# Optimization experiments

Measured on AMD Instinct MI355X. Metric: run time of the kernel, lower is better.

## Reference

```python
import jax, jax.numpy as jnp
import numpy as np
from numpy.lib.stride_tricks import sliding_window_view

# Static configuration matching init_kwargs
F_, H_, W_ = 2, 32, 32          # video_shape
K = 5                            # kernel_size (odd)
HEADS, DIM_HEAD = 8, 64
N = F_ * H_ * W_                 # number of video tokens (2048)
PAD = K // 2
INNER = HEADS * DIM_HEAD         # 512


def _neighbors():
    # Flattened token index at each (f,h,w); pad with sentinel N (out of bounds -> zeros / masked)
    idx = np.arange(N, dtype=np.int32).reshape(F_, H_, W_)
    padded = np.full((F_ + 2 * PAD, H_ + 2 * PAD, W_ + 2 * PAD), N, dtype=np.int32)
    padded[PAD:PAD + F_, PAD:PAD + H_, PAD:PAD + W_] = idx
    # sliding_window_view matches unfoldNd's kernel-offset ordering (kf, kh, kw row-major)
    return sliding_window_view(padded, (K, K, K)).reshape(N, K ** 3)


NBR = jnp.asarray(_neighbors())                                   # [N, K^3]
# causal: query i attends only to neighbors with index <= i; prepend BOS column (never masked)
CAUSAL = jnp.pad(jnp.arange(N)[:, None] < NBR, ((0, 0), (1, 0)))  # [N, K^3 + 1]


def setup_inputs() -> dict:
    key = jax.random.key(0)
    k1, k2, k3 = jax.random.split(key, 3)
    return {
        "x": jax.random.normal(k1, (1, N, INNER), jnp.float32),
        "w_qkv": jax.random.normal(k2, (INNER, 3 * INNER), jnp.float32) * 0.02,
        "w_out": jax.random.normal(k3, (INNER, INNER), jnp.float32) * 0.02,
        "b_out": jnp.zeros((INNER,), jnp.float32),
    }


def reference(x, w_qkv, w_out, b_out):
    b, n, dim = x.shape            # n == N
    bh = b * HEADS
    scale = DIM_HEAD ** -0.5

    xp = jnp.pad(x, ((0, 0), (0, 1), (0, 0)))        # pad one zero token at the end: [b, n+1, dim]
    qkv = xp @ w_qkv                                  # [b, n+1, 3*inner]
    q, kk, vv = jnp.split(qkv, 3, axis=-1)

    def split_heads(t):  # 'b n (h d) -> (b h) n d'
        return t.reshape(b, n + 1, HEADS, DIM_HEAD).transpose(0, 2, 1, 3).reshape(bh, n + 1, DIM_HEAD)

    q, kk, vv = map(split_heads, (q, kk, vv))
    q = q[:, 1:] * scale                              # drop BOS query: [bh, n, d]
    k_bos, kk = kk[:, :1], kk[:, 1:]                  # BOS kv + n spatial tokens
    v_bos, vv = vv[:, :1], vv[:, 1:]

    # Append a zero row so the sentinel index N gathers zeros (== unfold's zero padding)
    zero = jnp.zeros((bh, 1, DIM_HEAD), kk.dtype)
    kw = jnp.concatenate([kk, zero], axis=1)[:, NBR]  # [bh, n, K^3, d]
    vw = jnp.concatenate([vv, zero], axis=1)[:, NBR]

    bos_k = jnp.broadcast_to(k_bos[:, None], (bh, n, 1, DIM_HEAD))
    bos_v = jnp.broadcast_to(v_bos[:, None], (bh, n, 1, DIM_HEAD))
    kw = jnp.concatenate([bos_k, kw], axis=2)         # [bh, n, K^3+1, d]
    vw = jnp.concatenate([bos_v, vw], axis=2)

    sim = jnp.einsum('bid,bijd->bij', q, kw)          # [bh, n, K^3+1]
    sim = jnp.where(CAUSAL[:n], -jnp.finfo(sim.dtype).max, sim)
    attn = jax.nn.softmax(sim, axis=-1)
    out = jnp.einsum('bij,bijd->bid', attn, vw)       # [bh, n, d]

    out = jnp.concatenate([v_bos, out], axis=1)       # BOS output = its value: [bh, n+1, d]
    out = out.reshape(b, HEADS, n + 1, DIM_HEAD).transpose(0, 2, 1, 3).reshape(b, n + 1, INNER)
    return (out @ w_out + b_out)[:, :n]
```

## Files before the change

### kernel.cpp

```cpp
#include <hip/hip_runtime.h>
#include <hip/hip_bf16.h>

#define NTOK  2048
#define INNER 512
#define KDIM  512
#define QKVP  1536

typedef __attribute__((ext_vector_type(8))) short bf16x8;
typedef __attribute__((ext_vector_type(4))) float f32x4;

__device__ __forceinline__ unsigned short f2b(float f) {
  unsigned int u = __float_as_uint(f);
  return (unsigned short)((u + 0x7FFFu + ((u >> 16) & 1u)) >> 16);
}

__global__ __launch_bounds__(256) void prep_w(const float* __restrict__ w_qkv,
                                              const float* __restrict__ w_out,
                                              unsigned short* __restrict__ wqkvT,
                                              unsigned short* __restrict__ woutT) {
  __shared__ float tile[32][33];
  int b = blockIdx.x;
  const float* in; unsigned short* out; int K, N, bx, by;
  if (b < 768) { in = w_qkv; out = wqkvT; K = 512; N = 1536; bx = b % 48; by = b / 48; }
  else { b -= 768; in = w_out; out = woutT; K = 512; N = 512; bx = b & 15; by = b >> 4; }
  const int k0 = by * 32, n0 = bx * 32;
  const int r = threadIdx.x >> 3, c4 = (threadIdx.x & 7) * 4;
  float4 v = *(const float4*)(in + (size_t)(k0 + r) * N + n0 + c4);
  tile[r][c4 + 0] = v.x; tile[r][c4 + 1] = v.y;
  tile[r][c4 + 2] = v.z; tile[r][c4 + 3] = v.w;
  __syncthreads();
  ushort4 o;
  o.x = f2b(tile[c4 + 0][r]);
  o.y = f2b(tile[c4 + 1][r]);
  o.z = f2b(tile[c4 + 2][r]);
  o.w = f2b(tile[c4 + 3][r]);
  *(ushort4*)(out + (size_t)(n0 + r) * K + k0 + c4) = o;
}

__global__ __launch_bounds__(256, 2) void gemm_qkv(const float* __restrict__ x,
                                                   const unsigned short* __restrict__ Bt,
                                                   unsigned short* __restrict__ C) {
  constexpr int BM = 64, BN = 128, BK = 32, N = 1536, K = 512;
  __shared__ __align__(16) unsigned short As[BM * BK];
  __shared__ __align__(16) unsigned short Bs[BN * BK];
  const int tid = threadIdx.x, lane = tid & 63, wave = tid >> 6;
  const int m0 = blockIdx.y * BM, n0 = blockIdx.x * BN;
  const int wm = (wave >> 1) * 32, wn = (wave & 1) * 64;
  const int ar = tid >> 2, ac = (tid & 3) * 8;
  const int li0 = tid * 8, li1 = (256 + tid) * 8;
  const int br0 = li0 >> 5, bc0 = li0 & 31;
  const int br1 = li1 >> 5, bc1 = li1 & 31;
  const int fr = lane & 15, fk = (lane >> 4) * 8;

  f32x4 acc[2][4] = {};

  for (int k0 = 0; k0 < K; k0 += BK) {
    float4 a0 = *(const float4*)(x + (size_t)(m0 + ar) * K + k0 + ac);
    float4 a1 = *(const float4*)(x + (size_t)(m0 + ar) * K + k0 + ac + 4);
    bf16x8 av;
    av[0] = (short)f2b(a0.x); av[1] = (short)f2b(a0.y);
    av[2] = (short)f2b(a0.z); av[3] = (short)f2b(a0.w);
    av[4] = (short)f2b(a1.x); av[5] = (short)f2b(a1.y);
    av[6] = (short)f2b(a1.z); av[7] = (short)f2b(a1.w);
    *(bf16x8*)&As[ar * BK + ac] = av;
    *(bf16x8*)&Bs[li0] = *(const bf16x8*)(Bt + (size_t)(n0 + br0) * K + k0 + bc0);
    *(bf16x8*)&Bs[li1] = *(const bf16x8*)(Bt + (size_t)(n0 + br1) * K + k0 + bc1);
    __syncthreads();

    bf16x8 af[2], bfr[4];
#pragma unroll
    for (int i = 0; i < 2; ++i) af[i] = *(const bf16x8*)&As[(wm + i * 16 + fr) * BK + fk];
#pragma unroll
    for (int j = 0; j < 4; ++j) bfr[j] = *(const bf16x8*)&Bs[(wn + j * 16 + fr) * BK + fk];
#pragma unroll
    for (int i = 0; i < 2; ++i)
#pragma unroll
      for (int j = 0; j < 4; ++j)
        acc[i][j] = __builtin_amdgcn_mfma_f32_16x16x32_bf16(af[i], bfr[j], acc[i][j], 0, 0, 0);
    __syncthreads();
  }

  const int er = (lane >> 4) * 4, ec = lane & 15;
#pragma unroll
  for (int i = 0; i < 2; ++i)
#pragma unroll
    for (int j = 0; j < 4; ++j) {
      const int col = n0 + wn + j * 16 + ec;
#pragma unroll
      for (int r = 0; r < 4; ++r) {
        const int row = m0 + wm + i * 16 + er + r;
        C[(size_t)row * N + col] = f2b(acc[i][j][r]);
      }
    }
}

__global__ __launch_bounds__(256, 2) void gemm_out(const unsigned short* __restrict__ A,
                                                   const unsigned short* __restrict__ Bt,
                                                   const float* __restrict__ bias,
                                                   float* __restrict__ C) {
  constexpr int BM = 64, BN = 64, BK = 32, N = 512, K = 512;
  __shared__ __align__(16) unsigned short As[BM * BK];
  __shared__ __align__(16) unsigned short Bs[BN * BK];
  const int tid = threadIdx.x, lane = tid & 63, wave = tid >> 6;
  const int m0 = blockIdx.y * BM, n0 = blockIdx.x * BN;
  const int wm = (wave >> 1) * 32, wn = (wave & 1) * 32;
  const int r = tid >> 2, c = (tid & 3) * 8, li = tid * 8;
  const int fr = lane & 15, fk = (lane >> 4) * 8;

  f32x4 acc[2][2] = {};

  for (int k0 = 0; k0 < K; k0 += BK) {
    *(bf16x8*)&As[li] = *(const bf16x8*)(A + (size_t)(m0 + r) * K + k0 + c);
    *(bf16x8*)&Bs[li] = *(const bf16x8*)(Bt + (size_t)(n0 + r) * K + k0 + c);
    __syncthreads();
    bf16x8 af[2], bfr[2];
#pragma unroll
    for (int i = 0; i < 2; ++i) af[i] = *(const bf16x8*)&As[(wm + i * 16 + fr) * BK + fk];
#pragma unroll
    for (int j = 0; j < 2; ++j) bfr[j] = *(const bf16x8*)&Bs[(wn + j * 16 + fr) * BK + fk];
#pragma unroll
    for (int i = 0; i < 2; ++i)
#pragma unroll
      for (int j = 0; j < 2; ++j)
        acc[i][j] = __builtin_amdgcn_mfma_f32_16x16x32_bf16(af[i], bfr[j], acc[i][j], 0, 0, 0);
    __syncthreads();
  }

  const int er = (lane >> 4) * 4, ec = lane & 15;
#pragma unroll
  for (int i = 0; i < 2; ++i)
#pragma unroll
    for (int j = 0; j < 2; ++j) {
      const int col = n0 + wn + j * 16 + ec;
      const float b = bias[col];
#pragma unroll
      for (int rr = 0; rr < 4; ++rr) {
        const int row = m0 + wm + i * 16 + er + rr;
        C[(size_t)row * N + col] = acc[i][j][rr] + b;
      }
    }
}

__global__ __launch_bounds__(512) void attn_mfma(const unsigned short* __restrict__ qkv,
                                                 unsigned short* __restrict__ O) {
  __shared__ __align__(16) int list[192];
  __shared__ int cntS;
  __shared__ __align__(16) float mOd[4][16][72];
  __shared__ float mM[4][16], mL[4][16];

  const int tid = threadIdx.x;
  const int hg = blockIdx.y;

  if (blockIdx.x == 128) {
    if (tid < 256) O[hg * 256 + tid] = qkv[1024 + hg * 256 + tid];
    return;
  }
  const int pt = blockIdx.x;
  const int f  = pt >> 6;
  const int hh = (pt >> 1) & 31;
  const int w0 = (pt & 1) << 4;
  const int base_i = (f << 10) | (hh << 5) | w0;

  if (tid < 192) list[tid] = 0x7FFFFFFF;
  if (tid == 0) { list[0] = 0; cntS = 1; }
  __syncthreads();
  if (tid >= 1 && tid <= 160) {
    int cc = tid - 1;
    int p = cc / 20, wo = cc - p * 20;
    int ff = (p < 5) ? 0 : 1;
    int h2 = hh - 2 + ((p < 5) ? p : (p - 5));
    bool ok = (p < 5) ? ((f == 1) ? (h2 >= 0 && h2 <= 31) : (p <= 2 && h2 >= 0))
                      : (f == 1 && h2 >= 0);
    if (ok) {
      bool diag = (ff == f) && (h2 == hh);
      int wlo = max(0, w0 - 2);
      int whi = min(31, diag ? (w0 + 15) : (w0 + 17));
      int w2 = wlo + wo;
      if (w2 <= whi) {
        int pos = atomicAdd(&cntS, 1);
        list[pos] = ((ff << 10) | (h2 << 5) | w2) + 1;
      }
    }
  }
  __syncthreads();
  const int cnt  = cntS;
  const int nsub = (cnt + 15) >> 4;

  const int lane = tid & 63;
  const int wave = tid >> 6;
  const int hw   = wave >> 1;
  const int half = wave & 1;
  const int head = hg * 4 + hw;
  const int quad = lane >> 4;
  const int ec   = lane & 15;

  const int i_q = base_i + ec;
  const int tq  = min(i_q + 1, 2047);
  const unsigned short* qrow = qkv + (size_t)tq * QKVP + head * 64 + quad * 8;
  const bf16x8 qb0 = *(const bf16x8*)(qrow);
  const bf16x8 qb1 = *(const bf16x8*)(qrow + 32);

  f32x4 Od[4] = {{0,0,0,0},{0,0,0,0},{0,0,0,0},{0,0,0,0}};
  float m = -1e30f, l = 0.0f;

  for (int sub = half; sub < nsub; sub += 2) {
    const int base = sub * 16;
    const int tok_e = list[base + ec];
    const int4 tokv = *(const int4*)&list[base + quad * 4];
    const int tk[4] = {tokv.x, tokv.y, tokv.z, tokv.w};

    f32x4 S = {0, 0, 0, 0};
    {
      const int t0 = (tok_e > 2047) ? 0 : tok_e;
      const unsigned short* kr = qkv + (size_t)t0 * QKVP + 512 + head * 64 + quad * 8;
      const bf16x8 kf0 = *(const bf16x8*)(kr);
      const bf16x8 kf1 = *(const bf16x8*)(kr + 32);
      S = __builtin_amdgcn_mfma_f32_16x16x32_bf16(kf0, qb0, S, 0, 0, 0);
      S = __builtin_amdgcn_mfma_f32_16x16x32_bf16(kf1, qb1, S, 0, 0, 0);
    }

    float Sm[4];
#pragma unroll
    for (int r = 0; r < 4; ++r) {
      const int tok = tk[r];
      const int idx = tok - 1;
      const bool v = (tok == 0) ||
                     ((idx <= i_q) && ((unsigned)((idx & 31) - (w0 + ec) + 2) <= 4u));
      Sm[r] = v ? S[r] * 0.125f : -1e30f;
    }
    float mx = fmaxf(fmaxf(Sm[0], Sm[1]), fmaxf(Sm[2], Sm[3]));
    mx = fmaxf(mx, __shfl_xor(mx, 16, 64));
    mx = fmaxf(mx, __shfl_xor(mx, 32, 64));
    const float mn = fmaxf(m, mx);
    const float corr = __expf(m - mn);
    m = mn;
    const float p0 = __expf(Sm[0] - mn);
    const float p1 = __expf(Sm[1] - mn);
    const float p2 = __expf(Sm[2] - mn);
    const float p3 = __expf(Sm[3] - mn);
    float rs = (p0 + p1) + (p2 + p3);
    rs += __shfl_xor(rs, 16, 64);
    rs += __shfl_xor(rs, 32, 64);
    l = l * corr + rs;

    bf16x8 pf;
    pf[0] = (short)f2b(p0); pf[1] = (short)f2b(p1);
    pf[2] = (short)f2b(p2); pf[3] = (short)f2b(p3);
    pf[4] = 0; pf[5] = 0; pf[6] = 0; pf[7] = 0;

    const unsigned short* vp[4];
#pragma unroll
    for (int j = 0; j < 4; ++j) {
      const int tv = (tk[j] > 2047) ? 0 : tk[j];
      vp[j] = qkv + (size_t)tv * QKVP + 1024 + head * 64 + ec;
    }
#pragma unroll
    for (int dt = 0; dt < 4; ++dt) {
      bf16x8 vf;
#pragma unroll
      for (int j = 0; j < 4; ++j) vf[j] = (short)vp[j][dt * 16];
      vf[4] = 0; vf[5] = 0; vf[6] = 0; vf[7] = 0;
#pragma unroll
      for (int r = 0; r < 4; ++r) Od[dt][r] *= corr;
      Od[dt] = __builtin_amdgcn_mfma_f32_16x16x32_bf16(vf, pf, Od[dt], 0, 0, 0);
    }
  }

  if (half == 1) {
#pragma unroll
    for (int dt = 0; dt < 4; ++dt)
      *(f32x4*)&mOd[hw][ec][dt * 16 + quad * 4] = Od[dt];
    if (quad == 0) { mM[hw][ec] = m; mL[hw][ec] = l; }
  }
  __syncthreads();
  if (half == 0 && i_q <= 2046) {
    const float m1 = mM[hw][ec], l1 = mL[hw][ec];
    const float mm = fmaxf(m, m1);
    const float c0 = __expf(m - mm), c1 = __expf(m1 - mm);
    const float rl = 1.0f / (l * c0 + l1 * c1);
    unsigned short* ob = O + (size_t)(i_q + 1) * 512 + head * 64 + quad * 4;
#pragma unroll
    for (int dt = 0; dt < 4; ++dt) {
      const f32x4 o1 = *(const f32x4*)&mOd[hw][ec][dt * 16 + quad * 4];
      ushort4 u;
      u.x = f2b((Od[dt][0] * c0 + o1[0] * c1) * rl);
      u.y = f2b((Od[dt][1] * c0 + o1[1] * c1) * rl);
      u.z = f2b((Od[dt][2] * c0 + o1[2] * c1) * rl);
      u.w = f2b((Od[dt][3] * c0 + o1[3] * c1) * rl);
      *(ushort4*)(ob + dt * 16) = u;
    }
  }
}


extern "C" void kernel_launch(void* const* d_in, const int* in_sizes, int n_in,
                              void* d_out, int out_size, void* d_ws, size_t ws_size,
                              hipStream_t stream) {
  const float* x     = (const float*)d_in[0];
  const float* w_qkv = (const float*)d_in[1];
  const float* w_out = (const float*)d_in[2];
  const float* b_out = (const float*)d_in[3];
  float* out = (float*)d_out;

  char* ws = (char*)d_ws;
  unsigned short* qkvb  = (unsigned short*)(ws);
  unsigned short* wqkvT = (unsigned short*)(ws + 6291456);
  unsigned short* woutT = (unsigned short*)(ws + 7864320);
  unsigned short* Ob    = (unsigned short*)(ws + 8388608);

  hipLaunchKernelGGL(prep_w, dim3(1024), dim3(256), 0, stream, w_qkv, w_out, wqkvT, woutT);

  hipLaunchKernelGGL(gemm_qkv, dim3(12, 32), dim3(256), 0, stream, x, wqkvT, qkvb);

  hipLaunchKernelGGL(attn_mfma, dim3(129, 2), dim3(512), 0, stream, qkvb, Ob);

  hipLaunchKernelGGL(gemm_out, dim3(8, 32), dim3(256), 0, stream, Ob, woutT, b_out, out);
}
```

Measured before the change: 98.38 us.

## Precompute neighbor lists in prep, async LDS loads in GEMMs, smaller attention blocks

Moves the per-tile neighbor-list construction out of the attention kernel into the weight-prep kernel, which writes the lists and counts to workspace for the attention kernel to load. Both GEMMs now fill B tiles (and A tiles for the output GEMM) with global_load_lds direct-to-LDS copies. The attention grid changes from 129x2 blocks of 512 threads to 129x4 blocks of 256 threads, handling two heads per block instead of four. Together these aim to shorten the attention kernel's serial prologue, raise block count for occupancy, and cut register staging in the GEMMs. The costs are an extra global round trip for the lists and reliance on the async copy finishing before the barrier.

```diff
diff --git a/kernel.cpp b/kernel.cpp
--- a/kernel.cpp
+++ b/kernel.cpp
@@ -14,152 +14,46 @@
   return (unsigned short)((u + 0x7FFFu + ((u >> 16) & 1u)) >> 16);
 }
 
-__global__ __launch_bounds__(256) void prep_w(const float* __restrict__ w_qkv,
-                                              const float* __restrict__ w_out,
-                                              unsigned short* __restrict__ wqkvT,
-                                              unsigned short* __restrict__ woutT) {
+__device__ __forceinline__ void async_copy16(const unsigned short* g, unsigned short* l) {
+  __builtin_amdgcn_global_load_lds((const __attribute__((address_space(1))) void*)g,
+                                   (__attribute__((address_space(3))) void*)l, 16, 0, 0);
+}
+
+__global__ __launch_bounds__(256) void prep(const float* __restrict__ w_qkv,
+                                            const float* __restrict__ w_out,
+                                            unsigned short* __restrict__ wqkvT,
+                                            unsigned short* __restrict__ woutT,
+                                            int* __restrict__ glist,
+                                            int* __restrict__ gcnt) {
   __shared__ float tile[32][33];
+  __shared__ int list[192];
+  __shared__ int cntS;
+  const int tid = threadIdx.x;
   int b = blockIdx.x;
-  const float* in; unsigned short* out; int K, N, bx, by;
-  if (b < 768) { in = w_qkv; out = wqkvT; K = 512; N = 1536; bx = b % 48; by = b / 48; }
-  else { b -= 768; in = w_out; out = woutT; K = 512; N = 512; bx = b & 15; by = b >> 4; }
-  const int k0 = by * 32, n0 = bx * 32;
-  const int r = threadIdx.x >> 3, c4 = (threadIdx.x & 7) * 4;
-  float4 v = *(const float4*)(in + (size_t)(k0 + r) * N + n0 + c4);
-  tile[r][c4 + 0] = v.x; tile[r][c4 + 1] = v.y;
-  tile[r][c4 + 2] = v.z; tile[r][c4 + 3] = v.w;
-  __syncthreads();
-  ushort4 o;
-  o.x = f2b(tile[c4 + 0][r]);
-  o.y = f2b(tile[c4 + 1][r]);
-  o.z = f2b(tile[c4 + 2][r]);
-  o.w = f2b(tile[c4 + 3][r]);
-  *(ushort4*)(out + (size_t)(n0 + r) * K + k0 + c4) = o;
-}
-
-__global__ __launch_bounds__(256, 2) void gemm_qkv(const float* __restrict__ x,
-                                                   const unsigned short* __restrict__ Bt,
-                                                   unsigned short* __restrict__ C) {
-  constexpr int BM = 64, BN = 128, BK = 32, N = 1536, K = 512;
-  __shared__ __align__(16) unsigned short As[BM * BK];
-  __shared__ __align__(16) unsigned short Bs[BN * BK];
-  const int tid = threadIdx.x, lane = tid & 63, wave = tid >> 6;
-  const int m0 = blockIdx.y * BM, n0 = blockIdx.x * BN;
-  const int wm = (wave >> 1) * 32, wn = (wave & 1) * 64;
-  const int ar = tid >> 2, ac = (tid & 3) * 8;
-  const int li0 = tid * 8, li1 = (256 + tid) * 8;
-  const int br0 = li0 >> 5, bc0 = li0 & 31;
-  const int br1 = li1 >> 5, bc1 = li1 & 31;
-  const int fr = lane & 15, fk = (lane >> 4) * 8;
-
-  f32x4 acc[2][4] = {};
-
-  for (int k0 = 0; k0 < K; k0 += BK) {
-    float4 a0 = *(const float4*)(x + (size_t)(m0 + ar) * K + k0 + ac);
-    float4 a1 = *(const float4*)(x + (size_t)(m0 + ar) * K + k0 + ac + 4);
-    bf16x8 av;
-    av[0] = (short)f2b(a0.x); av[1] = (short)f2b(a0.y);
-    av[2] = (short)f2b(a0.z); av[3] = (short)f2b(a0.w);
-    av[4] = (short)f2b(a1.x); av[5] = (short)f2b(a1.y);
-    av[6] = (short)f2b(a1.z); av[7] = (short)f2b(a1.w);
-    *(bf16x8*)&As[ar * BK + ac] = av;
-    *(bf16x8*)&Bs[li0] = *(const bf16x8*)(Bt + (size_t)(n0 + br0) * K + k0 + bc0);
-    *(bf16x8*)&Bs[li1] = *(const bf16x8*)(Bt + (size_t)(n0 + br1) * K + k0 + bc1);
-    __syncthreads();
-
-    bf16x8 af[2], bfr[4];
-#pragma unroll
-    for (int i = 0; i < 2; ++i) af[i] = *(const bf16x8*)&As[(wm + i * 16 + fr) * BK + fk];
-#pragma unroll
-    for (int j = 0; j < 4; ++j) bfr[j] = *(const bf16x8*)&Bs[(wn + j * 16 + fr) * BK + fk];
-#pragma unroll
-    for (int i = 0; i < 2; ++i)
-#pragma unroll
-      for (int j = 0; j < 4; ++j)
-        acc[i][j] = __builtin_amdgcn_mfma_f32_16x16x32_bf16(af[i], bfr[j], acc[i][j], 0, 0, 0);
-    __syncthreads();
-  }
-
-  const int er = (lane >> 4) * 4, ec = lane & 15;
-#pragma unroll
-  for (int i = 0; i < 2; ++i)
-#pragma unroll
-    for (int j = 0; j < 4; ++j) {
-      const int col = n0 + wn + j * 16 + ec;
-#pragma unroll
-      for (int r = 0; r < 4; ++r) {
-        const int row = m0 + wm + i * 16 + er + r;
-        C[(size_t)row * N + col] = f2b(acc[i][j][r]);
-      }
-    }
-}
-
-__global__ __launch_bounds__(256, 2) void gemm_out(const unsigned short* __restrict__ A,
-                                                   const unsigned short* __restrict__ Bt,
-                                                   const float* __restrict__ bias,
-                                                   float* __restrict__ C) {
-  constexpr int BM = 64, BN = 64, BK = 32, N = 512, K = 512;
-  __shared__ __align__(16) unsigned short As[BM * BK];
-  __shared__ __align__(16) unsigned short Bs[BN * BK];
-  const int tid = threadIdx.x, lane = tid & 63, wave = tid >> 6;
-  const int m0 = blockIdx.y * BM, n0 = blockIdx.x * BN;
-  const int wm = (wave >> 1) * 32, wn = (wave & 1) * 32;
-  const int r = tid >> 2, c = (tid & 3) * 8, li = tid * 8;
-  const int fr = lane & 15, fk = (lane >> 4) * 8;
-
-  f32x4 acc[2][2] = {};
-
-  for (int k0 = 0; k0 < K; k0 += BK) {
-    *(bf16x8*)&As[li] = *(const bf16x8*)(A + (size_t)(m0 + r) * K + k0 + c);
-    *(bf16x8*)&Bs[li] = *(const bf16x8*)(Bt + (size_t)(n0 + r) * K + k0 + c);
-    __syncthreads();
-    bf16x8 af[2], bfr[2];
-#pragma unroll
-    for (int i = 0; i < 2; ++i) af[i] = *(const bf16x8*)&As[(wm + i * 16 + fr) * BK + fk];
-#pragma unroll
-    for (int j = 0; j < 2; ++j) bfr[j] = *(const bf16x8*)&Bs[(wn + j * 16 + fr) * BK + fk];
-#pragma unroll
-    for (int i = 0; i < 2; ++i)
-#pragma unroll
-      for (int j = 0; j < 2; ++j)
-        acc[i][j] = __builtin_amdgcn_mfma_f32_16x16x32_bf16(af[i], bfr[j], acc[i][j], 0, 0, 0);
-    __syncthreads();
-  }
-
-  const int er = (lane >> 4) * 4, ec = lane & 15;
-#pragma unroll
-  for (int i = 0; i < 2; ++i)
-#pragma unroll
-    for (int j = 0; j < 2; ++j) {
-      const int col = n0 + wn + j * 16 + ec;
-      const float b = bias[col];
-#pragma unroll
-      for (int rr = 0; rr < 4; ++rr) {
-        const int row = m0 + wm + i * 16 + er + rr;
-        C[(size_t)row * N + col] = acc[i][j][rr] + b;
-      }
-    }
-}
-
-__global__ __launch_bounds__(512) void attn_mfma(const unsigned short* __restrict__ qkv,
-                                                 unsigned short* __restrict__ O) {
-  __shared__ __align__(16) int list[192];
-  __shared__ int cntS;
-  __shared__ __align__(16) float mOd[4][16][72];
-  __shared__ float mM[4][16], mL[4][16];
-
-  const int tid = threadIdx.x;
-  const int hg = blockIdx.y;
-
-  if (blockIdx.x == 128) {
-    if (tid < 256) O[hg * 256 + tid] = qkv[1024 + hg * 256 + tid];
+
+  if (b < 1024) {
+    const float* in; unsigned short* out; int K, N, bx, by;
+    if (b < 768) { in = w_qkv; out = wqkvT; K = 512; N = 1536; bx = b % 48; by = b / 48; }
+    else { int bb = b - 768; in = w_out; out = woutT; K = 512; N = 512; bx = bb & 15; by = bb >> 4; }
+    const int k0 = by * 32, n0 = bx * 32;
+    const int r = tid >> 3, c4 = (tid & 7) * 4;
+    float4 v = *(const float4*)(in + (size_t)(k0 + r) * N + n0 + c4);
+    tile[r][c4 + 0] = v.x; tile[r][c4 + 1] = v.y;
+    tile[r][c4 + 2] = v.z; tile[r][c4 + 3] = v.w;
+    __syncthreads();
+    ushort4 o;
+    o.x = f2b(tile[c4 + 0][r]);
+    o.y = f2b(tile[c4 + 1][r]);
+    o.z = f2b(tile[c4 + 2][r]);
+    o.w = f2b(tile[c4 + 3][r]);
+    *(ushort4*)(out + (size_t)(n0 + r) * K + k0 + c4) = o;
     return;
   }
-  const int pt = blockIdx.x;
+
+  const int pt = b - 1024;
   const int f  = pt >> 6;
   const int hh = (pt >> 1) & 31;
   const int w0 = (pt & 1) << 4;
-  const int base_i = (f << 10) | (hh << 5) | w0;
 
   if (tid < 192) list[tid] = 0x7FFFFFFF;
   if (tid == 0) { list[0] = 0; cntS = 1; }
@@ -183,6 +77,141 @@
     }
   }
   __syncthreads();
+  if (tid < 192) glist[pt * 192 + tid] = list[tid];
+  if (tid == 0) gcnt[pt] = cntS;
+}
+
+__global__ __launch_bounds__(256, 2) void gemm_qkv(const float* __restrict__ x,
+                                                   const unsigned short* __restrict__ Bt,
+                                                   unsigned short* __restrict__ C) {
+  constexpr int BK = 32, N = 1536, K = 512;
+  __shared__ __align__(16) unsigned short As[64 * BK];
+  __shared__ __align__(16) unsigned short Bs[128 * BK];
+  const int tid = threadIdx.x, lane = tid & 63, wave = tid >> 6;
+  const int m0 = blockIdx.y * 64, n0 = blockIdx.x * 128;
+  const int wm = (wave >> 1) * 32, wn = (wave & 1) * 64;
+  const int ar = tid >> 2, ac = (tid & 3) * 8;
+  const int bl0 = ((wave * 2 + 0) * 64 + lane) * 8;
+  const int bl1 = ((wave * 2 + 1) * 64 + lane) * 8;
+  const int bn0 = bl0 >> 5, bk0 = bl0 & 31;
+  const int bn1 = bl1 >> 5, bk1 = bl1 & 31;
+  const int fr = lane & 15, fk = (lane >> 4) * 8;
+
+  f32x4 acc[2][4] = {};
+
+  for (int k0 = 0; k0 < K; k0 += BK) {
+    async_copy16(Bt + (size_t)(n0 + bn0) * K + k0 + bk0, &Bs[bl0]);
+    async_copy16(Bt + (size_t)(n0 + bn1) * K + k0 + bk1, &Bs[bl1]);
+    const float* ap = x + (size_t)(m0 + ar) * K + k0 + ac;
+    float4 a0 = *(const float4*)(ap);
+    float4 a1 = *(const float4*)(ap + 4);
+    bf16x8 av;
+    av[0] = (short)f2b(a0.x); av[1] = (short)f2b(a0.y);
+    av[2] = (short)f2b(a0.z); av[3] = (short)f2b(a0.w);
+    av[4] = (short)f2b(a1.x); av[5] = (short)f2b(a1.y);
+    av[6] = (short)f2b(a1.z); av[7] = (short)f2b(a1.w);
+    *(bf16x8*)&As[ar * BK + ac] = av;
+    __syncthreads();
+
+    bf16x8 af[2], bfr[4];
+#pragma unroll
+    for (int i = 0; i < 2; ++i) af[i] = *(const bf16x8*)&As[(wm + i * 16 + fr) * BK + fk];
+#pragma unroll
+    for (int j = 0; j < 4; ++j) bfr[j] = *(const bf16x8*)&Bs[(wn + j * 16 + fr) * BK + fk];
+#pragma unroll
+    for (int i = 0; i < 2; ++i)
+#pragma unroll
+      for (int j = 0; j < 4; ++j)
+        acc[i][j] = __builtin_amdgcn_mfma_f32_16x16x32_bf16(af[i], bfr[j], acc[i][j], 0, 0, 0);
+    __syncthreads();
+  }
+
+  const int er = (lane >> 4) * 4, ec = lane & 15;
+#pragma unroll
+  for (int i = 0; i < 2; ++i)
+#pragma unroll
+    for (int j = 0; j < 4; ++j) {
+      const int col = n0 + wn + j * 16 + ec;
+#pragma unroll
+      for (int r = 0; r < 4; ++r) {
+        const int row = m0 + wm + i * 16 + er + r;
+        C[(size_t)row * N + col] = f2b(acc[i][j][r]);
+      }
+    }
+}
+
+__global__ __launch_bounds__(256, 2) void gemm_out(const unsigned short* __restrict__ A,
+                                                   const unsigned short* __restrict__ Bt,
+                                                   const float* __restrict__ bias,
+                                                   float* __restrict__ C) {
+  constexpr int BK = 32, N = 512, K = 512;
+  __shared__ __align__(16) unsigned short As[64 * BK];
+  __shared__ __align__(16) unsigned short Bs[64 * BK];
+  const int tid = threadIdx.x, lane = tid & 63, wave = tid >> 6;
+  const int m0 = blockIdx.y * 64, n0 = blockIdx.x * 64;
+  const int wm = (wave >> 1) * 32, wn = (wave & 1) * 32;
+  const int li = tid * 8, r = li >> 5, c = li & 31;
+  const int fr = lane & 15, fk = (lane >> 4) * 8;
+
+  f32x4 acc[2][2] = {};
+
+  for (int k0 = 0; k0 < K; k0 += BK) {
+    async_copy16(A  + (size_t)(m0 + r) * K + k0 + c, &As[li]);
+    async_copy16(Bt + (size_t)(n0 + r) * K + k0 + c, &Bs[li]);
+    __syncthreads();
+    bf16x8 af[2], bfr[2];
+#pragma unroll
+    for (int i = 0; i < 2; ++i) af[i] = *(const bf16x8*)&As[(wm + i * 16 + fr) * BK + fk];
+#pragma unroll
+    for (int j = 0; j < 2; ++j) bfr[j] = *(const bf16x8*)&Bs[(wn + j * 16 + fr) * BK + fk];
+#pragma unroll
+    for (int i = 0; i < 2; ++i)
+#pragma unroll
+      for (int j = 0; j < 2; ++j)
+        acc[i][j] = __builtin_amdgcn_mfma_f32_16x16x32_bf16(af[i], bfr[j], acc[i][j], 0, 0, 0);
+    __syncthreads();
+  }
+
+  const int er = (lane >> 4) * 4, ec = lane & 15;
+#pragma unroll
+  for (int i = 0; i < 2; ++i)
+#pragma unroll
+    for (int j = 0; j < 2; ++j) {
+      const int col = n0 + wn + j * 16 + ec;
+      const float b = bias[col];
+#pragma unroll
+      for (int rr = 0; rr < 4; ++rr) {
+        const int row = m0 + wm + i * 16 + er + rr;
+        C[(size_t)row * N + col] = acc[i][j][rr] + b;
+      }
+    }
+}
+
+__global__ __launch_bounds__(256) void attn_mfma(const unsigned short* __restrict__ qkv,
+                                                 const int* __restrict__ glist,
+                                                 const int* __restrict__ gcnt,
+                                                 unsigned short* __restrict__ O) {
+  __shared__ __align__(16) int list[192];
+  __shared__ __align__(16) float mOd[2][16][72];
+  __shared__ float mM[2][16], mL[2][16];
+  __shared__ int cntS;
+
+  const int tid = threadIdx.x;
+  const int hp = blockIdx.y;
+
+  if (blockIdx.x == 128) {
+    if (tid < 128) O[hp * 128 + tid] = qkv[1024 + hp * 128 + tid];
+    return;
+  }
+  const int pt = blockIdx.x;
+  const int f  = pt >> 6;
+  const int hh = (pt >> 1) & 31;
+  const int w0 = (pt & 1) << 4;
+  const int base_i = (f << 10) | (hh << 5) | w0;
+
+  if (tid < 192) list[tid] = glist[pt * 192 + tid];
+  if (tid == 0) cntS = gcnt[pt];
+  __syncthreads();
   const int cnt  = cntS;
   const int nsub = (cnt + 15) >> 4;
 
@@ -190,7 +219,7 @@
   const int wave = tid >> 6;
   const int hw   = wave >> 1;
   const int half = wave & 1;
-  const int head = hg * 4 + hw;
+  const int head = hp * 2 + hw;
   const int quad = lane >> 4;
   const int ec   = lane & 15;
 
@@ -307,12 +336,15 @@
   unsigned short* wqkvT = (unsigned short*)(ws + 6291456);
   unsigned short* woutT = (unsigned short*)(ws + 7864320);
   unsigned short* Ob    = (unsigned short*)(ws + 8388608);
-
-  hipLaunchKernelGGL(prep_w, dim3(1024), dim3(256), 0, stream, w_qkv, w_out, wqkvT, woutT);
+  int*            glist = (int*)(ws + 10485760);
+  int*            gcnt  = (int*)(ws + 10584064);
+
+  hipLaunchKernelGGL(prep, dim3(1152), dim3(256), 0, stream,
+                     w_qkv, w_out, wqkvT, woutT, glist, gcnt);
 
   hipLaunchKernelGGL(gemm_qkv, dim3(12, 32), dim3(256), 0, stream, x, wqkvT, qkvb);
 
-  hipLaunchKernelGGL(attn_mfma, dim3(129, 2), dim3(512), 0, stream, qkvb, Ob);
+  hipLaunchKernelGGL(attn_mfma, dim3(129, 4), dim3(256), 0, stream, qkvb, glist, gcnt, Ob);
 
   hipLaunchKernelGGL(gemm_out, dim3(8, 32), dim3(256), 0, stream, Ob, woutT, b_out, out);
 }
```

Result: no change. 99.36 us (+1.0%).
